# Performance work log

Measured on AMD Instinct MI355X. Metric: run time of the kernel, lower is better.

## Reference

```python
import jax, jax.numpy as jnp
import numpy as np

R, B, S, U, D = 4, 2048, 10, 20000, 128

def setup_inputs() -> dict:
    key = jax.random.key(0)
    k1, k2 = jax.random.split(key)
    neigh_idx = jax.random.randint(k1, (R, B, S), 0, U)  # sampled neighbor ids (indices into unique node list)
    embed = jax.random.normal(k2, (U, D), dtype=jnp.float32)  # features(unique_nodes_list)
    return {"neigh_idx": neigh_idx, "embed": embed}

def reference(neigh_idx, embed):
    r, b, s = neigh_idx.shape
    u, d = embed.shape
    # Dense 0/1 mask [R, B, U]: mask[rel, row, col] = 1 (set, duplicates collapse like a set)
    rel_ix = jnp.arange(r)[:, None, None]
    row_ix = jnp.arange(b)[None, :, None]
    mask = jnp.zeros((r, b, u), dtype=embed.dtype).at[rel_ix, row_ix, neigh_idx].set(1.0)
    mask = mask.reshape(r * b, u)
    num_neigh = mask.sum(axis=1, keepdims=True)
    mask = jnp.where(num_neigh != 0, mask / num_neigh, jnp.zeros_like(mask))
    # Dense matmul with embedding matrix, as in the original
    to_feats = mask @ embed  # [R*B, D]
    return to_feats
```

## Files before the change

### kernel.cpp

```cpp
#include <hip/hip_runtime.h>


#define RR 4
#define BB 2048
#define SS 10
#define UU 20000
#define DD 128

__global__ __launch_bounds__(256) void mean_agg_kernel(
    const int* __restrict__ neigh_idx,
    const float* __restrict__ embed,
    float* __restrict__ out)
{
    const int t   = blockIdx.x * blockDim.x + threadIdx.x;
    const int row = t >> 5;
    const int c4  = t & 31;
    if (row >= RR * BB) return;

    int id[SS];
    const int* ip = neigh_idx + row * SS;
    #pragma unroll
    for (int j = 0; j < SS; ++j) id[j] = ip[j];

    float4 acc = make_float4(0.f, 0.f, 0.f, 0.f);
    int cnt = 0;
    #pragma unroll
    for (int j = 0; j < SS; ++j) {
        bool dup = false;
        #pragma unroll
        for (int i = 0; i < j; ++i) dup = dup || (id[i] == id[j]);
        if (!dup) {
            ++cnt;
            const float4 v = *reinterpret_cast<const float4*>(
                embed + (size_t)id[j] * DD + (c4 << 2));
            acc.x += v.x; acc.y += v.y; acc.z += v.z; acc.w += v.w;
        }
    }
    const float inv = 1.0f / (float)cnt;
    acc.x *= inv; acc.y *= inv; acc.z *= inv; acc.w *= inv;

    reinterpret_cast<float4*>(out)[row * 32 + c4] = acc;
}

extern "C" void kernel_launch(void* const* d_in, const int* in_sizes, int n_in,
                              void* d_out, int out_size, void* d_ws, size_t ws_size,
                              hipStream_t stream) {
    const int*   neigh_idx = (const int*)d_in[0];
    const float* embed     = (const float*)d_in[1];
    float*       out       = (float*)d_out;

    const int rows    = RR * BB;
    const int threads = rows * 32;
    const int block   = 256;
    const int grid    = (threads + block - 1) / block;

    mean_agg_kernel<<<grid, block, 0, stream>>>(neigh_idx, embed, out);
}
```

Before: 10.97 us.

## Remap threads to 64-row by 64-byte column chunks and use nontemporal stores

Changes the thread mapping so each block covers 64 rows times one 16-float column chunk, with 4 threads per row and 8 column chunks spread across blocks, instead of 8 full rows per block. This groups blocks that read the same column slice of the embedding table, which may improve cache locality. Output writes become nontemporal stores to avoid polluting cache. The trade-off is that each wavefront now issues 64-byte segments across 16 rows rather than 512-byte contiguous rows, which could hurt coalescing.

Measured after the change: 9.871 us. 1.11x faster.

```diff
diff --git a/kernel.cpp b/kernel.cpp
--- a/kernel.cpp
+++ b/kernel.cpp
@@ -6,23 +6,33 @@
 #define SS 10
 #define UU 20000
 #define DD 128
+#define ROWS (RR * BB)
+#define NCHUNK 8
+
+typedef float vfloat4 __attribute__((ext_vector_type(4)));
 
 __global__ __launch_bounds__(256) void mean_agg_kernel(
     const int* __restrict__ neigh_idx,
     const float* __restrict__ embed,
     float* __restrict__ out)
 {
-    const int t   = blockIdx.x * blockDim.x + threadIdx.x;
-    const int row = t >> 5;
-    const int c4  = t & 31;
-    if (row >= RR * BB) return;
+    const int chunk  = blockIdx.x & (NCHUNK - 1);
+    const int group  = blockIdx.x >> 3;
+    const int tid    = threadIdx.x;
+    const int rlocal = tid >> 2;
+    const int c4l    = tid & 3;
+    const int row    = group * 64 + rlocal;
+    const int col4   = chunk * 4 + c4l;
 
     int id[SS];
     const int* ip = neigh_idx + row * SS;
     #pragma unroll
     for (int j = 0; j < SS; ++j) id[j] = ip[j];
 
-    float4 acc = make_float4(0.f, 0.f, 0.f, 0.f);
+    const vfloat4* __restrict__ esrc =
+        reinterpret_cast<const vfloat4*>(embed) + col4;
+
+    vfloat4 acc = (vfloat4){0.f, 0.f, 0.f, 0.f};
     int cnt = 0;
     #pragma unroll
     for (int j = 0; j < SS; ++j) {
@@ -31,15 +41,13 @@
         for (int i = 0; i < j; ++i) dup = dup || (id[i] == id[j]);
         if (!dup) {
             ++cnt;
-            const float4 v = *reinterpret_cast<const float4*>(
-                embed + (size_t)id[j] * DD + (c4 << 2));
-            acc.x += v.x; acc.y += v.y; acc.z += v.z; acc.w += v.w;
+            acc += esrc[(size_t)id[j] * (DD / 4)];
         }
     }
-    const float inv = 1.0f / (float)cnt;
-    acc.x *= inv; acc.y *= inv; acc.z *= inv; acc.w *= inv;
+    acc *= (1.0f / (float)cnt);
 
-    reinterpret_cast<float4*>(out)[row * 32 + c4] = acc;
+    __builtin_nontemporal_store(
+        acc, reinterpret_cast<vfloat4*>(out) + (size_t)row * 32 + col4);
 }
 
 extern "C" void kernel_launch(void* const* d_in, const int* in_sizes, int n_in,
@@ -49,10 +57,8 @@
     const float* embed     = (const float*)d_in[1];
     float*       out       = (float*)d_out;
 
-    const int rows    = RR * BB;
-    const int threads = rows * 32;
-    const int block   = 256;
-    const int grid    = (threads + block - 1) / block;
+    const int block = 256;
+    const int grid  = (ROWS / 64) * NCHUNK;
 
     mean_agg_kernel<<<grid, block, 0, stream>>>(neigh_idx, embed, out);
 }
```
